# Optimization experiments

Measured on AMD Instinct MI355X. Metric: run time of the kernel, lower is better.

The kernel has to match this reference:

```python
import jax, jax.numpy as jnp
import numpy as np

N_NODES = 50000
N_EDGES = 600000
IN_C, HID_C, OUT_C = 128, 128, 64
NUM_GRAPHS = 512


def sage_conv(x, src, dst, Wl, bl, Wr):
    """PyG SAGEConv (aggr='mean'): out = mean_{j->i} x_j @ Wl + bl + x_i @ Wr."""
    n = x.shape[0]
    msg = x[src]  # [E, d] gather
    agg = jax.ops.segment_sum(msg, dst, num_segments=n)
    deg = jax.ops.segment_sum(jnp.ones((src.shape[0], 1), x.dtype), dst, num_segments=n)
    agg = agg / jnp.maximum(deg, 1.0)
    return agg @ Wl + bl + x @ Wr


def setup_inputs() -> dict:
    key = jax.random.key(0)
    ks = jax.random.split(key, 12)
    x = jax.random.normal(ks[0], (N_NODES, IN_C), dtype=jnp.float32)
    edge_index = jax.random.randint(ks[1], (2, N_EDGES), 0, N_NODES, dtype=jnp.int32)
    cluster = jnp.sort(jax.random.randint(ks[2], (N_NODES,), 0, NUM_GRAPHS, dtype=jnp.int32))
    def lin(k, din, dout):
        s = 1.0 / np.sqrt(din)
        return (jax.random.uniform(k, (din, dout), jnp.float32, -s, s))
    return {
        "x": x, "edge_index": edge_index, "cluster": cluster,
        "Wl0": lin(ks[3], IN_C, HID_C), "bl0": jnp.zeros((HID_C,), jnp.float32), "Wr0": lin(ks[4], IN_C, HID_C),
        "Wl1": lin(ks[5], HID_C, HID_C), "bl1": jnp.zeros((HID_C,), jnp.float32), "Wr1": lin(ks[6], HID_C, HID_C),
        "Wl2": lin(ks[7], HID_C, OUT_C), "bl2": jnp.zeros((OUT_C,), jnp.float32), "Wr2": lin(ks[8], HID_C, OUT_C),
    }


def reference(x, edge_index, cluster, Wl0, bl0, Wr0, Wl1, bl1, Wr1, Wl2, bl2, Wr2):
    src, dst = edge_index[0], edge_index[1]
    out = None
    # hidden SAGEConv layers + relu (dropout inactive in eval)
    for Wl, bl, Wr in ((Wl0, bl0, Wr0), (Wl1, bl1, Wr1)):
        out = sage_conv(x, src, dst, Wl, bl, Wr)
        x = jax.nn.relu(out)
    # scatter-mean graph pooling over cluster ids
    gsum = jax.ops.segment_sum(x, cluster, num_segments=NUM_GRAPHS)
    gcnt = jax.ops.segment_sum(jnp.ones((x.shape[0], 1), x.dtype), cluster, num_segments=NUM_GRAPHS)
    g = gsum / jnp.maximum(gcnt, 1.0)
    # final conv + log-softmax over classes
    xf = sage_conv(x, src, dst, Wl2, bl2, Wr2)
    return (jax.nn.log_softmax(xf, axis=-1), out, g)
```

## Files before the change

kernel.cpp:

```cpp
#include <hip/hip_runtime.h>
#include <math.h>

#define NN 50000
#define NE 600000
#define NG 512

typedef unsigned int u32;
typedef unsigned short u16;

typedef __attribute__((ext_vector_type(8))) short bf16x8;
typedef __attribute__((ext_vector_type(4))) float f32x4;
typedef __attribute__((ext_vector_type(4))) unsigned int u32x4;

__device__ __forceinline__ float bf2f(u16 u) {
  return __uint_as_float(((u32)u) << 16);
}
__device__ __forceinline__ u16 f2bf(float f) {
  u32 u = __float_as_uint(f);
  u32 lsb = (u >> 16) & 1u;
  u += 0x7fffu + lsb;
  return (u16)(u >> 16);
}

__global__ __launch_bounds__(256)
void deg_count_k(const int* __restrict__ ei, int* __restrict__ deg) {
  int e = blockIdx.x * 256 + threadIdx.x;
  if (e >= NE) return;
  atomicAdd(&deg[ei[NE + e]], 1);
}

__global__ __launch_bounds__(256)
void scan1_k(const int* __restrict__ deg, int* __restrict__ bsum) {
  __shared__ int s[256];
  int idx = blockIdx.x * 256 + threadIdx.x;
  int v = (idx < NN) ? deg[idx] : 0;
  s[threadIdx.x] = v;
  __syncthreads();
  for (int off = 128; off > 0; off >>= 1) {
    if (threadIdx.x < off) s[threadIdx.x] += s[threadIdx.x + off];
    __syncthreads();
  }
  if (threadIdx.x == 0) bsum[blockIdx.x] = s[0];
}

__global__ __launch_bounds__(256)
void scan2_k(const int* __restrict__ bsum, int* __restrict__ bofs, int* __restrict__ row_ptr) {
  __shared__ int s[256];
  int t = threadIdx.x;
  int v = (t < 196) ? bsum[t] : 0;
  s[t] = v;
  __syncthreads();
  for (int off = 1; off < 256; off <<= 1) {
    int add = (t >= off) ? s[t - off] : 0;
    __syncthreads();
    s[t] += add;
    __syncthreads();
  }
  if (t < 196) bofs[t] = s[t] - v;
  if (t == 0) row_ptr[NN] = NE;
}

__global__ __launch_bounds__(256)
void scan3_k(const int* __restrict__ deg, const int* __restrict__ bofs,
             int* __restrict__ row_ptr, int* __restrict__ cursor) {
  __shared__ int s[256];
  int idx = blockIdx.x * 256 + threadIdx.x;
  int t = threadIdx.x;
  int v = (idx < NN) ? deg[idx] : 0;
  s[t] = v;
  __syncthreads();
  for (int off = 1; off < 256; off <<= 1) {
    int add = (t >= off) ? s[t - off] : 0;
    __syncthreads();
    s[t] += add;
    __syncthreads();
  }
  if (idx < NN) {
    int p = bofs[blockIdx.x] + s[t] - v;
    row_ptr[idx] = p;
    cursor[idx] = p;
  }
}

__global__ __launch_bounds__(256)
void fill_k(const int* __restrict__ ei, int* __restrict__ cursor, int* __restrict__ perm) {
  int e = blockIdx.x * 256 + threadIdx.x;
  if (e >= NE) return;
  int pos = atomicAdd(&cursor[ei[NE + e]], 1);
  perm[pos] = ei[e];
}

__global__ __launch_bounds__(256)
void cast_k(const float* __restrict__ x, u32* __restrict__ xb) {
  int tid = blockIdx.x * 256 + threadIdx.x;
  float2 v = ((const float2*)x)[tid];
  xb[tid] = (u32)f2bf(v.x) | ((u32)f2bf(v.y) << 16);
}

__global__ __launch_bounds__(256)
void castW_k(const float* __restrict__ Wl, const float* __restrict__ Wr,
             u16* __restrict__ WbT, int ncols) {
  int t = blockIdx.x * 256 + threadIdx.x;
  int n = t >> 8;
  int k = t & 255;
  if (n >= ncols) return;
  float v = (k < 128) ? Wl[k * ncols + n] : Wr[(k - 128) * ncols + n];
  int c = k >> 3, e = k & 7;
  WbT[n * 256 + (((c ^ (n & 7)) << 3) | e)] = f2bf(v);
}

__global__ __launch_bounds__(256)
void gather4_k(const u16* __restrict__ xb, const int* __restrict__ row_ptr,
               const int* __restrict__ perm, u16* __restrict__ aggb) {
  int wave = threadIdx.x >> 6;
  int lane = threadIdx.x & 63;
  int grp  = lane >> 4;
  int l16  = lane & 15;
  int n = (blockIdx.x * 4 + wave) * 4 + grp;
  int beg = row_ptr[n];
  int cnt = row_ptr[n + 1] - beg;
  int beg_s = min(beg, NE - 1);
  int last = max(cnt - 1, 0);
  int m = max(cnt, __shfl_xor(cnt, 16));
  int jmax = max(m, __shfl_xor(m, 32));
  float acc[8];
#pragma unroll
  for (int i = 0; i < 8; i++) acc[i] = 0.f;
  const u32x4* xv = (const u32x4*)xb;
  for (int base = 0; base < jmax; base += 8) {
    int idx[8];
#pragma unroll
    for (int j = 0; j < 8; j++) idx[j] = perm[beg_s + min(base + j, last)];
    u32x4 v[8];
#pragma unroll
    for (int j = 0; j < 8; j++) v[j] = xv[(size_t)idx[j] * 16 + l16];
#pragma unroll
    for (int j = 0; j < 8; j++) {
      bool live = (base + j) < cnt;
#pragma unroll
      for (int w = 0; w < 4; w++) {
        u32 u = v[j][w];
        acc[2 * w]     += live ? __uint_as_float(u << 16) : 0.f;
        acc[2 * w + 1] += live ? __uint_as_float(u & 0xffff0000u) : 0.f;
      }
    }
  }
  float inv = 1.0f / fmaxf((float)cnt, 1.0f);
  u32x4 o;
#pragma unroll
  for (int w = 0; w < 4; w++)
    o[w] = (u32)f2bf(acc[2 * w] * inv) | ((u32)f2bf(acc[2 * w + 1] * inv) << 16);
  ((u32x4*)aggb)[(size_t)n * 16 + l16] = o;
}

template<int NCOL, bool WRITE_PRE, bool SOFTMAX>
__global__ __launch_bounds__(256)
void sage_mfma_v2_k(const u16* __restrict__ aggb, const u16* __restrict__ xbin,
                    const u16* __restrict__ WbT, const float* __restrict__ bl,
                    u16* __restrict__ xb_out, float* __restrict__ out_pre,
                    float* __restrict__ out_f) {
  __shared__ u16 wsh[NCOL * 256];
  int tid = threadIdx.x;

  {
    const u32x4* g = (const u32x4*)WbT;
    u32x4* l = (u32x4*)wsh;
#pragma unroll
    for (int i = 0; i < NCOL / 8; i++)
      l[tid + i * 256] = g[tid + i * 256];
  }
  __syncthreads();

  int wave = tid >> 6;
  int lane = tid & 63;
  int quad = lane >> 4;
  int m16  = lane & 15;
  int r0 = blockIdx.x * 64 + wave * 16;

  int rowA = min(r0 + m16, NN - 1);
  const u16* pa = aggb + (size_t)rowA * 128 + quad * 8;
  const u16* px = xbin + (size_t)rowA * 128 + quad * 8;
  bf16x8 a[8];
#pragma unroll
  for (int j = 0; j < 4; j++) a[j]     = *(const bf16x8*)(pa + j * 32);
#pragma unroll
  for (int j = 0; j < 4; j++) a[4 + j] = *(const bf16x8*)(px + j * 32);

  constexpr int NT = NCOL / 16;
  f32x4 acc[NT];
#pragma unroll
  for (int nt = 0; nt < NT; nt++) acc[nt] = (f32x4){0.f, 0.f, 0.f, 0.f};

  int swz = m16 & 7;
#pragma unroll
  for (int ks = 0; ks < 8; ks++) {
#pragma unroll
    for (int nt = 0; nt < NT; nt++) {
      const u16* bp = wsh + (nt * 16 + m16) * 256 + (((quad + ks * 4) ^ swz) << 3);
      bf16x8 b = *(const bf16x8*)bp;
      acc[nt] = __builtin_amdgcn_mfma_f32_16x16x32_bf16(a[ks], b, acc[nt], 0, 0, 0);
    }
  }

  float bv[NT];
#pragma unroll
  for (int nt = 0; nt < NT; nt++) bv[nt] = bl[nt * 16 + m16];

  int rbase = r0 + quad * 4;
  if (!SOFTMAX) {
#pragma unroll
    for (int r = 0; r < 4; r++) {
      int row = rbase + r;
      if (row < NN) {
#pragma unroll
        for (int nt = 0; nt < NT; nt++) {
          int col = nt * 16 + m16;
          float v = acc[nt][r] + bv[nt];
          if (WRITE_PRE) out_pre[(size_t)row * NCOL + col] = v;
          xb_out[(size_t)row * NCOL + col] = f2bf(fmaxf(v, 0.f));
        }
      }
    }
  } else {
#pragma unroll
    for (int r = 0; r < 4; r++) {
      float v0 = acc[0][r] + bv[0];
      float v1 = acc[1][r] + bv[1];
      float v2 = acc[2][r] + bv[2];
      float v3 = acc[3][r] + bv[3];
      float m = fmaxf(fmaxf(v0, v1), fmaxf(v2, v3));
#pragma unroll
      for (int mk = 1; mk <= 8; mk <<= 1) m = fmaxf(m, __shfl_xor(m, mk));
      float s = __expf(v0 - m) + __expf(v1 - m) + __expf(v2 - m) + __expf(v3 - m);
#pragma unroll
      for (int mk = 1; mk <= 8; mk <<= 1) s += __shfl_xor(s, mk);
      float ls = m + __logf(s);
      int row = rbase + r;
      if (row < NN) {
        float* orow = out_f + (size_t)row * 64;
        orow[m16]      = v0 - ls;
        orow[16 + m16] = v1 - ls;
        orow[32 + m16] = v2 - ls;
        orow[48 + m16] = v3 - ls;
      }
    }
  }
}

__global__ __launch_bounds__(256)
void pool_seg_k(const u16* __restrict__ xb, const int* __restrict__ cluster,
                float* __restrict__ g) {
  __shared__ float sh[256];
  int gid = blockIdx.x;
  int t = threadIdx.x;
  int ch = t & 127;
  int half = t >> 7;
  int lo = 0, hi = NN;
  while (lo < hi) { int mid = (lo + hi) >> 1; if (cluster[mid] < gid) lo = mid + 1; else hi = mid; }
  int beg = lo;
  hi = NN;
  while (lo < hi) { int mid = (lo + hi) >> 1; if (cluster[mid] < gid + 1) lo = mid + 1; else hi = mid; }
  int end = lo;
  float s0 = 0.f, s1 = 0.f;
  int n = beg + half;
  for (; n + 2 < end; n += 4) {
    s0 += bf2f(xb[(size_t)n * 128 + ch]);
    s1 += bf2f(xb[(size_t)(n + 2) * 128 + ch]);
  }
  if (n < end) s0 += bf2f(xb[(size_t)n * 128 + ch]);
  sh[t] = s0 + s1;
  __syncthreads();
  if (t < 128) {
    float s = sh[t] + sh[t + 128];
    g[gid * 128 + t] = s / fmaxf((float)(end - beg), 1.0f);
  }
}

extern "C" void kernel_launch(void* const* d_in, const int* in_sizes, int n_in,
                              void* d_out, int out_size, void* d_ws, size_t ws_size,
                              hipStream_t stream) {
  const float* x   = (const float*)d_in[0];
  const int*   ei  = (const int*)d_in[1];
  const int*   cl  = (const int*)d_in[2];
  const float* Wl0 = (const float*)d_in[3];
  const float* bl0 = (const float*)d_in[4];
  const float* Wr0 = (const float*)d_in[5];
  const float* Wl1 = (const float*)d_in[6];
  const float* bl1 = (const float*)d_in[7];
  const float* Wr1 = (const float*)d_in[8];
  const float* Wl2 = (const float*)d_in[9];
  const float* bl2 = (const float*)d_in[10];
  const float* Wr2 = (const float*)d_in[11];
  float* out = (float*)d_out;

  char* ws = (char*)d_ws;
  u16*   xb0     = (u16*)  (ws);
  u16*   xb1     = (u16*)  (ws + 12800000);
  u16*   xb2     = (u16*)  (ws + 25600000);
  u16*   aggb    = (u16*)  (ws + 38400000);
  u16*   WbT0    = (u16*)  (ws + 51200000);
  u16*   WbT1    = (u16*)  (ws + 51265536);
  u16*   WbT2    = (u16*)  (ws + 51331072);
  int*   deg     = (int*)  (ws + 51363840);
  int*   row_ptr = (int*)  (ws + 51564032);
  int*   cursor  = (int*)  (ws + 51764736);
  int*   perm    = (int*)  (ws + 51964736);
  int*   bsum    = (int*)  (ws + 54364736);
  int*   bofs    = (int*)  (ws + 54365568);

  float* out_lsm = out;
  float* out_pre = out + 3200000;
  float* out_g   = out + 9600000;

  hipMemsetAsync(deg, 0, 200000, stream);
  deg_count_k<<<2344, 256, 0, stream>>>(ei, deg);
  scan1_k<<<196, 256, 0, stream>>>(deg, bsum);
  scan2_k<<<1, 256, 0, stream>>>(bsum, bofs, row_ptr);
  scan3_k<<<196, 256, 0, stream>>>(deg, bofs, row_ptr, cursor);
  fill_k<<<2344, 256, 0, stream>>>(ei, cursor, perm);

  cast_k<<<12500, 256, 0, stream>>>(x, (u32*)xb0);
  castW_k<<<128, 256, 0, stream>>>(Wl0, Wr0, WbT0, 128);
  castW_k<<<128, 256, 0, stream>>>(Wl1, Wr1, WbT1, 128);
  castW_k<<<64, 256, 0, stream>>>(Wl2, Wr2, WbT2, 64);

  gather4_k<<<3125, 256, 0, stream>>>(xb0, row_ptr, perm, aggb);
  sage_mfma_v2_k<128, false, false><<<782, 256, 0, stream>>>(aggb, xb0, WbT0, bl0, xb1, nullptr, nullptr);

  gather4_k<<<3125, 256, 0, stream>>>(xb1, row_ptr, perm, aggb);
  sage_mfma_v2_k<128, true, false><<<782, 256, 0, stream>>>(aggb, xb1, WbT1, bl1, xb2, out_pre, nullptr);

  pool_seg_k<<<NG, 256, 0, stream>>>(xb2, cl, out_g);

  gather4_k<<<3125, 256, 0, stream>>>(xb2, row_ptr, perm, aggb);
  sage_mfma_v2_k<64, false, true><<<782, 256, 0, stream>>>(aggb, xb2, WbT2, bl2, nullptr, nullptr, out_lsm);
}
```

Measured before the change: 293.3 us.

## Bucket CSR edges by source chunk to improve gather locality

Builds the CSR with each destination's edges sub-bucketed into four source-index ranges. The gather kernel then walks the chunks in order so concurrent waves touch a narrower band of feature rows, aiming for better cache hit rates. The cost is a 4x larger degree/scan array, a bigger scan, and per-chunk loop overhead with padding to groups of eight. This padding may waste many loads given the low per-chunk degree.

```diff
diff --git a/kernel.cpp b/kernel.cpp
--- a/kernel.cpp
+++ b/kernel.cpp
@@ -4,6 +4,10 @@
 #define NN 50000
 #define NE 600000
 #define NG 512
+#define NCHUNK 4
+#define CHUNK 12500
+#define NBUCK (NN * NCHUNK)
+#define NSCAN_BLK 782
 
 typedef unsigned int u32;
 typedef unsigned short u16;
@@ -26,14 +30,16 @@
 void deg_count_k(const int* __restrict__ ei, int* __restrict__ deg) {
   int e = blockIdx.x * 256 + threadIdx.x;
   if (e >= NE) return;
-  atomicAdd(&deg[ei[NE + e]], 1);
+  u32 src = (u32)ei[e];
+  int bucket = ei[NE + e] * NCHUNK + (int)(src / CHUNK);
+  atomicAdd(&deg[bucket], 1);
 }
 
 __global__ __launch_bounds__(256)
 void scan1_k(const int* __restrict__ deg, int* __restrict__ bsum) {
   __shared__ int s[256];
   int idx = blockIdx.x * 256 + threadIdx.x;
-  int v = (idx < NN) ? deg[idx] : 0;
+  int v = (idx < NBUCK) ? deg[idx] : 0;
   s[threadIdx.x] = v;
   __syncthreads();
   for (int off = 128; off > 0; off >>= 1) {
@@ -43,21 +49,21 @@
   if (threadIdx.x == 0) bsum[blockIdx.x] = s[0];
 }
 
-__global__ __launch_bounds__(256)
+__global__ __launch_bounds__(1024)
 void scan2_k(const int* __restrict__ bsum, int* __restrict__ bofs, int* __restrict__ row_ptr) {
-  __shared__ int s[256];
+  __shared__ int s[1024];
   int t = threadIdx.x;
-  int v = (t < 196) ? bsum[t] : 0;
+  int v = (t < NSCAN_BLK) ? bsum[t] : 0;
   s[t] = v;
   __syncthreads();
-  for (int off = 1; off < 256; off <<= 1) {
+  for (int off = 1; off < 1024; off <<= 1) {
     int add = (t >= off) ? s[t - off] : 0;
     __syncthreads();
     s[t] += add;
     __syncthreads();
   }
-  if (t < 196) bofs[t] = s[t] - v;
-  if (t == 0) row_ptr[NN] = NE;
+  if (t < NSCAN_BLK) bofs[t] = s[t] - v;
+  if (t == 0) row_ptr[NBUCK] = NE;
 }
 
 __global__ __launch_bounds__(256)
@@ -66,7 +72,7 @@
   __shared__ int s[256];
   int idx = blockIdx.x * 256 + threadIdx.x;
   int t = threadIdx.x;
-  int v = (idx < NN) ? deg[idx] : 0;
+  int v = (idx < NBUCK) ? deg[idx] : 0;
   s[t] = v;
   __syncthreads();
   for (int off = 1; off < 256; off <<= 1) {
@@ -75,7 +81,7 @@
     s[t] += add;
     __syncthreads();
   }
-  if (idx < NN) {
+  if (idx < NBUCK) {
     int p = bofs[blockIdx.x] + s[t] - v;
     row_ptr[idx] = p;
     cursor[idx] = p;
@@ -86,8 +92,10 @@
 void fill_k(const int* __restrict__ ei, int* __restrict__ cursor, int* __restrict__ perm) {
   int e = blockIdx.x * 256 + threadIdx.x;
   if (e >= NE) return;
-  int pos = atomicAdd(&cursor[ei[NE + e]], 1);
-  perm[pos] = ei[e];
+  u32 src = (u32)ei[e];
+  int bucket = ei[NE + e] * NCHUNK + (int)(src / CHUNK);
+  int pos = atomicAdd(&cursor[bucket], 1);
+  perm[pos] = (int)src;
 }
 
 __global__ __launch_bounds__(256)
@@ -117,35 +125,38 @@
   int grp  = lane >> 4;
   int l16  = lane & 15;
   int n = (blockIdx.x * 4 + wave) * 4 + grp;
-  int beg = row_ptr[n];
-  int cnt = row_ptr[n + 1] - beg;
-  int beg_s = min(beg, NE - 1);
-  int last = max(cnt - 1, 0);
-  int m = max(cnt, __shfl_xor(cnt, 16));
-  int jmax = max(m, __shfl_xor(m, 32));
   float acc[8];
 #pragma unroll
   for (int i = 0; i < 8; i++) acc[i] = 0.f;
   const u32x4* xv = (const u32x4*)xb;
-  for (int base = 0; base < jmax; base += 8) {
-    int idx[8];
-#pragma unroll
-    for (int j = 0; j < 8; j++) idx[j] = perm[beg_s + min(base + j, last)];
-    u32x4 v[8];
-#pragma unroll
-    for (int j = 0; j < 8; j++) v[j] = xv[(size_t)idx[j] * 16 + l16];
-#pragma unroll
-    for (int j = 0; j < 8; j++) {
-      bool live = (base + j) < cnt;
-#pragma unroll
-      for (int w = 0; w < 4; w++) {
-        u32 u = v[j][w];
-        acc[2 * w]     += live ? __uint_as_float(u << 16) : 0.f;
-        acc[2 * w + 1] += live ? __uint_as_float(u & 0xffff0000u) : 0.f;
+  int tot = row_ptr[n * NCHUNK + NCHUNK] - row_ptr[n * NCHUNK];
+  for (int c = 0; c < NCHUNK; c++) {
+    int b0 = row_ptr[n * NCHUNK + c];
+    int cnt = row_ptr[n * NCHUNK + c + 1] - b0;
+    int beg_s = min(b0, NE - 1);
+    int last = max(cnt - 1, 0);
+    int m = max(cnt, __shfl_xor(cnt, 16));
+    int jmax = max(m, __shfl_xor(m, 32));
+    for (int base = 0; base < jmax; base += 8) {
+      int idx[8];
+#pragma unroll
+      for (int j = 0; j < 8; j++) idx[j] = perm[beg_s + min(base + j, last)];
+      u32x4 v[8];
+#pragma unroll
+      for (int j = 0; j < 8; j++) v[j] = xv[(size_t)idx[j] * 16 + l16];
+#pragma unroll
+      for (int j = 0; j < 8; j++) {
+        bool live = (base + j) < cnt;
+#pragma unroll
+        for (int w = 0; w < 4; w++) {
+          u32 u = v[j][w];
+          acc[2 * w]     += live ? __uint_as_float(u << 16) : 0.f;
+          acc[2 * w + 1] += live ? __uint_as_float(u & 0xffff0000u) : 0.f;
+        }
       }
     }
   }
-  float inv = 1.0f / fmaxf((float)cnt, 1.0f);
+  float inv = 1.0f / fmaxf((float)tot, 1.0f);
   u32x4 o;
 #pragma unroll
   for (int w = 0; w < 4; w++)
@@ -302,21 +313,21 @@
   u16*   WbT1    = (u16*)  (ws + 51265536);
   u16*   WbT2    = (u16*)  (ws + 51331072);
   int*   deg     = (int*)  (ws + 51363840);
-  int*   row_ptr = (int*)  (ws + 51564032);
-  int*   cursor  = (int*)  (ws + 51764736);
-  int*   perm    = (int*)  (ws + 51964736);
-  int*   bsum    = (int*)  (ws + 54364736);
-  int*   bofs    = (int*)  (ws + 54365568);
+  int*   row_ptr = (int*)  (ws + 52163840);
+  int*   perm    = (int*)  (ws + 52963968);
+  int*   bsum    = (int*)  (ws + 55363968);
+  int*   bofs    = (int*)  (ws + 55367168);
+  int*   cursor  = deg;
 
   float* out_lsm = out;
   float* out_pre = out + 3200000;
   float* out_g   = out + 9600000;
 
-  hipMemsetAsync(deg, 0, 200000, stream);
+  hipMemsetAsync(deg, 0, NBUCK * 4, stream);
   deg_count_k<<<2344, 256, 0, stream>>>(ei, deg);
-  scan1_k<<<196, 256, 0, stream>>>(deg, bsum);
-  scan2_k<<<1, 256, 0, stream>>>(bsum, bofs, row_ptr);
-  scan3_k<<<196, 256, 0, stream>>>(deg, bofs, row_ptr, cursor);
+  scan1_k<<<NSCAN_BLK, 256, 0, stream>>>(deg, bsum);
+  scan2_k<<<1, 1024, 0, stream>>>(bsum, bofs, row_ptr);
+  scan3_k<<<NSCAN_BLK, 256, 0, stream>>>(deg, bofs, row_ptr, cursor);
   fill_k<<<2344, 256, 0, stream>>>(ei, cursor, perm);
 
   cast_k<<<12500, 256, 0, stream>>>(x, (u32*)xb0);
```

New measurement: 315.8 us. 1.08x slower.

## Transform-before-aggregate in final layer and use wave-per-node edge gather

Applied to the files above, without the earlier changes.

The final SAGE layer now applies Wl2 to node features first (128->64 GEMM), then gathers and averages the 64-wide projected rows, so edge traffic per neighbour is halved. The right-hand term and log-softmax are computed in a separate kernel that adds the aggregated projection. The gather kernel is restructured to give one wave per node, with lane groups splitting edges and a cross-lane shuffle reduction, instead of four nodes per wave padded to the longest neighbour list. This adds an extra kernel launch and a bf16 rounding of the projected features before averaging, which changes numerics slightly.

```diff
diff --git a/kernel.cpp b/kernel.cpp
--- a/kernel.cpp
+++ b/kernel.cpp
@@ -110,63 +110,76 @@
 }
 
 __global__ __launch_bounds__(256)
-void gather4_k(const u16* __restrict__ xb, const int* __restrict__ row_ptr,
-               const int* __restrict__ perm, u16* __restrict__ aggb) {
+void castW64_k(const float* __restrict__ W, u16* __restrict__ WT) {
+  int t = blockIdx.x * 256 + threadIdx.x;
+  int n = t >> 7;
+  int k = t & 127;
+  float v = W[k * 64 + n];
+  int c = k >> 3, e = k & 7;
+  WT[n * 128 + (((c ^ (n & 7)) << 3) | e)] = f2bf(v);
+}
+
+template<int CH>
+__global__ __launch_bounds__(256)
+void gather_w_k(const u16* __restrict__ xb, const int* __restrict__ row_ptr,
+                const int* __restrict__ perm, u16* __restrict__ aggb) {
+  constexpr int CK = CH / 8;
+  constexpr int GR = 64 / CK;
   int wave = threadIdx.x >> 6;
   int lane = threadIdx.x & 63;
-  int grp  = lane >> 4;
-  int l16  = lane & 15;
-  int n = (blockIdx.x * 4 + wave) * 4 + grp;
+  int grp  = lane / CK;
+  int li   = lane & (CK - 1);
+  int n = blockIdx.x * 4 + wave;
   int beg = row_ptr[n];
   int cnt = row_ptr[n + 1] - beg;
   int beg_s = min(beg, NE - 1);
   int last = max(cnt - 1, 0);
-  int m = max(cnt, __shfl_xor(cnt, 16));
-  int jmax = max(m, __shfl_xor(m, 32));
   float acc[8];
 #pragma unroll
   for (int i = 0; i < 8; i++) acc[i] = 0.f;
   const u32x4* xv = (const u32x4*)xb;
-  for (int base = 0; base < jmax; base += 8) {
-    int idx[8];
-#pragma unroll
-    for (int j = 0; j < 8; j++) idx[j] = perm[beg_s + min(base + j, last)];
-    u32x4 v[8];
-#pragma unroll
-    for (int j = 0; j < 8; j++) v[j] = xv[(size_t)idx[j] * 16 + l16];
-#pragma unroll
-    for (int j = 0; j < 8; j++) {
-      bool live = (base + j) < cnt;
-#pragma unroll
-      for (int w = 0; w < 4; w++) {
-        u32 u = v[j][w];
-        acc[2 * w]     += live ? __uint_as_float(u << 16) : 0.f;
-        acc[2 * w + 1] += live ? __uint_as_float(u & 0xffff0000u) : 0.f;
-      }
-    }
+  for (int base = 0; base < cnt; base += 2 * GR) {
+    int i0 = perm[beg_s + min(base + grp, last)];
+    int i1 = perm[beg_s + min(base + GR + grp, last)];
+    u32x4 v0 = xv[(size_t)i0 * CK + li];
+    u32x4 v1 = xv[(size_t)i1 * CK + li];
+    bool a0 = (base + grp) < cnt;
+    bool a1 = (base + GR + grp) < cnt;
+#pragma unroll
+    for (int w = 0; w < 4; w++) {
+      acc[2 * w]     += a0 ? __uint_as_float(v0[w] << 16) : 0.f;
+      acc[2 * w + 1] += a0 ? __uint_as_float(v0[w] & 0xffff0000u) : 0.f;
+      acc[2 * w]     += a1 ? __uint_as_float(v1[w] << 16) : 0.f;
+      acc[2 * w + 1] += a1 ? __uint_as_float(v1[w] & 0xffff0000u) : 0.f;
+    }
+  }
+#pragma unroll
+  for (int off = CK; off < 64; off <<= 1) {
+#pragma unroll
+    for (int i = 0; i < 8; i++) acc[i] += __shfl_xor(acc[i], off);
   }
   float inv = 1.0f / fmaxf((float)cnt, 1.0f);
-  u32x4 o;
-#pragma unroll
-  for (int w = 0; w < 4; w++)
-    o[w] = (u32)f2bf(acc[2 * w] * inv) | ((u32)f2bf(acc[2 * w + 1] * inv) << 16);
-  ((u32x4*)aggb)[(size_t)n * 16 + l16] = o;
-}
-
-template<int NCOL, bool WRITE_PRE, bool SOFTMAX>
+  if (lane < CK) {
+    u32x4 o;
+#pragma unroll
+    for (int w = 0; w < 4; w++)
+      o[w] = (u32)f2bf(acc[2 * w] * inv) | ((u32)f2bf(acc[2 * w + 1] * inv) << 16);
+    ((u32x4*)aggb)[(size_t)n * CK + li] = o;
+  }
+}
+
+template<bool WRITE_PRE>
 __global__ __launch_bounds__(256)
 void sage_mfma_v2_k(const u16* __restrict__ aggb, const u16* __restrict__ xbin,
                     const u16* __restrict__ WbT, const float* __restrict__ bl,
-                    u16* __restrict__ xb_out, float* __restrict__ out_pre,
-                    float* __restrict__ out_f) {
-  __shared__ u16 wsh[NCOL * 256];
+                    u16* __restrict__ xb_out, float* __restrict__ out_pre) {
+  __shared__ u16 wsh[128 * 256];
   int tid = threadIdx.x;
-
   {
     const u32x4* g = (const u32x4*)WbT;
     u32x4* l = (u32x4*)wsh;
 #pragma unroll
-    for (int i = 0; i < NCOL / 8; i++)
+    for (int i = 0; i < 16; i++)
       l[tid + i * 256] = g[tid + i * 256];
   }
   __syncthreads();
@@ -186,63 +199,162 @@
 #pragma unroll
   for (int j = 0; j < 4; j++) a[4 + j] = *(const bf16x8*)(px + j * 32);
 
-  constexpr int NT = NCOL / 16;
-  f32x4 acc[NT];
-#pragma unroll
-  for (int nt = 0; nt < NT; nt++) acc[nt] = (f32x4){0.f, 0.f, 0.f, 0.f};
+  f32x4 acc[8];
+#pragma unroll
+  for (int nt = 0; nt < 8; nt++) acc[nt] = (f32x4){0.f, 0.f, 0.f, 0.f};
 
   int swz = m16 & 7;
 #pragma unroll
   for (int ks = 0; ks < 8; ks++) {
 #pragma unroll
-    for (int nt = 0; nt < NT; nt++) {
+    for (int nt = 0; nt < 8; nt++) {
       const u16* bp = wsh + (nt * 16 + m16) * 256 + (((quad + ks * 4) ^ swz) << 3);
       bf16x8 b = *(const bf16x8*)bp;
       acc[nt] = __builtin_amdgcn_mfma_f32_16x16x32_bf16(a[ks], b, acc[nt], 0, 0, 0);
     }
   }
 
-  float bv[NT];
-#pragma unroll
-  for (int nt = 0; nt < NT; nt++) bv[nt] = bl[nt * 16 + m16];
+  float bv[8];
+#pragma unroll
+  for (int nt = 0; nt < 8; nt++) bv[nt] = bl[nt * 16 + m16];
 
   int rbase = r0 + quad * 4;
-  if (!SOFTMAX) {
-#pragma unroll
-    for (int r = 0; r < 4; r++) {
-      int row = rbase + r;
-      if (row < NN) {
-#pragma unroll
-        for (int nt = 0; nt < NT; nt++) {
-          int col = nt * 16 + m16;
-          float v = acc[nt][r] + bv[nt];
-          if (WRITE_PRE) out_pre[(size_t)row * NCOL + col] = v;
-          xb_out[(size_t)row * NCOL + col] = f2bf(fmaxf(v, 0.f));
-        }
+#pragma unroll
+  for (int r = 0; r < 4; r++) {
+    int row = rbase + r;
+    if (row < NN) {
+#pragma unroll
+      for (int nt = 0; nt < 8; nt++) {
+        int col = nt * 16 + m16;
+        float v = acc[nt][r] + bv[nt];
+        if (WRITE_PRE) out_pre[(size_t)row * 128 + col] = v;
+        xb_out[(size_t)row * 128 + col] = f2bf(fmaxf(v, 0.f));
       }
     }
-  } else {
-#pragma unroll
-    for (int r = 0; r < 4; r++) {
-      float v0 = acc[0][r] + bv[0];
-      float v1 = acc[1][r] + bv[1];
-      float v2 = acc[2][r] + bv[2];
-      float v3 = acc[3][r] + bv[3];
-      float m = fmaxf(fmaxf(v0, v1), fmaxf(v2, v3));
-#pragma unroll
-      for (int mk = 1; mk <= 8; mk <<= 1) m = fmaxf(m, __shfl_xor(m, mk));
-      float s = __expf(v0 - m) + __expf(v1 - m) + __expf(v2 - m) + __expf(v3 - m);
-#pragma unroll
-      for (int mk = 1; mk <= 8; mk <<= 1) s += __shfl_xor(s, mk);
-      float ls = m + __logf(s);
-      int row = rbase + r;
-      if (row < NN) {
-        float* orow = out_f + (size_t)row * 64;
-        orow[m16]      = v0 - ls;
-        orow[16 + m16] = v1 - ls;
-        orow[32 + m16] = v2 - ls;
-        orow[48 + m16] = v3 - ls;
-      }
+  }
+}
+
+__global__ __launch_bounds__(256)
+void gemm64_k(const u16* __restrict__ xbin, const u16* __restrict__ WT,
+              u16* __restrict__ yb) {
+  __shared__ u16 wsh[64 * 128];
+  int tid = threadIdx.x;
+  {
+    const u32x4* g = (const u32x4*)WT;
+    u32x4* l = (u32x4*)wsh;
+#pragma unroll
+    for (int i = 0; i < 4; i++)
+      l[tid + i * 256] = g[tid + i * 256];
+  }
+  __syncthreads();
+
+  int wave = tid >> 6;
+  int lane = tid & 63;
+  int quad = lane >> 4;
+  int m16  = lane & 15;
+  int r0 = blockIdx.x * 64 + wave * 16;
+
+  int rowA = min(r0 + m16, NN - 1);
+  const u16* px = xbin + (size_t)rowA * 128 + quad * 8;
+  bf16x8 a[4];
+#pragma unroll
+  for (int j = 0; j < 4; j++) a[j] = *(const bf16x8*)(px + j * 32);
+
+  f32x4 acc[4];
+#pragma unroll
+  for (int nt = 0; nt < 4; nt++) acc[nt] = (f32x4){0.f, 0.f, 0.f, 0.f};
+
+  int swz = m16 & 7;
+#pragma unroll
+  for (int ks = 0; ks < 4; ks++) {
+#pragma unroll
+    for (int nt = 0; nt < 4; nt++) {
+      const u16* bp = wsh + (nt * 16 + m16) * 128 + (((ks * 4 + quad) ^ swz) << 3);
+      bf16x8 b = *(const bf16x8*)bp;
+      acc[nt] = __builtin_amdgcn_mfma_f32_16x16x32_bf16(a[ks], b, acc[nt], 0, 0, 0);
+    }
+  }
+
+  int rbase = r0 + quad * 4;
+#pragma unroll
+  for (int r = 0; r < 4; r++) {
+    int row = rbase + r;
+    if (row < NN) {
+#pragma unroll
+      for (int nt = 0; nt < 4; nt++)
+        yb[(size_t)row * 64 + nt * 16 + m16] = f2bf(acc[nt][r]);
+    }
+  }
+}
+
+__global__ __launch_bounds__(256)
+void sage64f_k(const u16* __restrict__ aggy, const u16* __restrict__ xbin,
+               const u16* __restrict__ WT, const float* __restrict__ bl,
+               float* __restrict__ out) {
+  __shared__ u16 wsh[64 * 128];
+  int tid = threadIdx.x;
+  {
+    const u32x4* g = (const u32x4*)WT;
+    u32x4* l = (u32x4*)wsh;
+#pragma unroll
+    for (int i = 0; i < 4; i++)
+      l[tid + i * 256] = g[tid + i * 256];
+  }
+  __syncthreads();
+
+  int wave = tid >> 6;
+  int lane = tid & 63;
+  int quad = lane >> 4;
+  int m16  = lane & 15;
+  int r0 = blockIdx.x * 64 + wave * 16;
+
+  int rowA = min(r0 + m16, NN - 1);
+  const u16* px = xbin + (size_t)rowA * 128 + quad * 8;
+  bf16x8 a[4];
+#pragma unroll
+  for (int j = 0; j < 4; j++) a[j] = *(const bf16x8*)(px + j * 32);
+
+  f32x4 acc[4];
+#pragma unroll
+  for (int nt = 0; nt < 4; nt++) acc[nt] = (f32x4){0.f, 0.f, 0.f, 0.f};
+
+  int swz = m16 & 7;
+#pragma unroll
+  for (int ks = 0; ks < 4; ks++) {
+#pragma unroll
+    for (int nt = 0; nt < 4; nt++) {
+      const u16* bp = wsh + (nt * 16 + m16) * 128 + (((ks * 4 + quad) ^ swz) << 3);
+      bf16x8 b = *(const bf16x8*)bp;
+      acc[nt] = __builtin_amdgcn_mfma_f32_16x16x32_bf16(a[ks], b, acc[nt], 0, 0, 0);
+    }
+  }
+
+  float bv[4];
+#pragma unroll
+  for (int nt = 0; nt < 4; nt++) bv[nt] = bl[nt * 16 + m16];
+
+  int rbase = r0 + quad * 4;
+#pragma unroll
+  for (int r = 0; r < 4; r++) {
+    int row = rbase + r;
+    int rs = min(row, NN - 1);
+    float v0 = acc[0][r] + bv[0] + bf2f(aggy[(size_t)rs * 64 + m16]);
+    float v1 = acc[1][r] + bv[1] + bf2f(aggy[(size_t)rs * 64 + 16 + m16]);
+    float v2 = acc[2][r] + bv[2] + bf2f(aggy[(size_t)rs * 64 + 32 + m16]);
+    float v3 = acc[3][r] + bv[3] + bf2f(aggy[(size_t)rs * 64 + 48 + m16]);
+    float m = fmaxf(fmaxf(v0, v1), fmaxf(v2, v3));
+#pragma unroll
+    for (int mk = 1; mk <= 8; mk <<= 1) m = fmaxf(m, __shfl_xor(m, mk));
+    float s = __expf(v0 - m) + __expf(v1 - m) + __expf(v2 - m) + __expf(v3 - m);
+#pragma unroll
+    for (int mk = 1; mk <= 8; mk <<= 1) s += __shfl_xor(s, mk);
+    float ls = m + __logf(s);
+    if (row < NN) {
+      float* orow = out + (size_t)row * 64;
+      orow[m16]      = v0 - ls;
+      orow[16 + m16] = v1 - ls;
+      orow[32 + m16] = v2 - ls;
+      orow[48 + m16] = v3 - ls;
     }
   }
 }
@@ -298,9 +410,12 @@
   u16*   xb1     = (u16*)  (ws + 12800000);
   u16*   xb2     = (u16*)  (ws + 25600000);
   u16*   aggb    = (u16*)  (ws + 38400000);
+  u16*   y2      = aggb;
+  u16*   aggy    = (u16*)  (ws + 38400000 + 6400000);
   u16*   WbT0    = (u16*)  (ws + 51200000);
   u16*   WbT1    = (u16*)  (ws + 51265536);
-  u16*   WbT2    = (u16*)  (ws + 51331072);
+  u16*   WlT2    = (u16*)  (ws + 51331072);
+  u16*   WrT2    = (u16*)  (ws + 51347456);
   int*   deg     = (int*)  (ws + 51363840);
   int*   row_ptr = (int*)  (ws + 51564032);
   int*   cursor  = (int*)  (ws + 51764736);
@@ -322,16 +437,18 @@
   cast_k<<<12500, 256, 0, stream>>>(x, (u32*)xb0);
   castW_k<<<128, 256, 0, stream>>>(Wl0, Wr0, WbT0, 128);
   castW_k<<<128, 256, 0, stream>>>(Wl1, Wr1, WbT1, 128);
-  castW_k<<<64, 256, 0, stream>>>(Wl2, Wr2, WbT2, 64);
-
-  gather4_k<<<3125, 256, 0, stream>>>(xb0, row_ptr, perm, aggb);
-  sage_mfma_v2_k<128, false, false><<<782, 256, 0, stream>>>(aggb, xb0, WbT0, bl0, xb1, nullptr, nullptr);
-
-  gather4_k<<<3125, 256, 0, stream>>>(xb1, row_ptr, perm, aggb);
-  sage_mfma_v2_k<128, true, false><<<782, 256, 0, stream>>>(aggb, xb1, WbT1, bl1, xb2, out_pre, nullptr);
+  castW64_k<<<32, 256, 0, stream>>>(Wl2, WlT2);
+  castW64_k<<<32, 256, 0, stream>>>(Wr2, WrT2);
+
+  gather_w_k<128><<<12500, 256, 0, stream>>>(xb0, row_ptr, perm, aggb);
+  sage_mfma_v2_k<false><<<782, 256, 0, stream>>>(aggb, xb0, WbT0, bl0, xb1, nullptr);
+
+  gather_w_k<128><<<12500, 256, 0, stream>>>(xb1, row_ptr, perm, aggb);
+  sage_mfma_v2_k<true><<<782, 256, 0, stream>>>(aggb, xb1, WbT1, bl1, xb2, out_pre);
 
   pool_seg_k<<<NG, 256, 0, stream>>>(xb2, cl, out_g);
 
-  gather4_k<<<3125, 256, 0, stream>>>(xb2, row_ptr, perm, aggb);
-  sage_mfma_v2_k<64, false, true><<<782, 256, 0, stream>>>(aggb, xb2, WbT2, bl2, nullptr, nullptr, out_lsm);
-}
+  gemm64_k<<<782, 256, 0, stream>>>(xb2, WlT2, y2);
+  gather_w_k<64><<<12500, 256, 0, stream>>>(y2, row_ptr, perm, aggy);
+  sage64f_k<<<782, 256, 0, stream>>>(aggy, xb2, WrT2, bl2, out_lsm);
+}
```

Measured after the change: 301.6 us. +2.8%, slower.
